# Optimization experiments

Hardware: AMD Instinct MI355X
Metric: run time of the kernel (lower is better)

Reference implementation:

```python
import jax, jax.numpy as jnp
import numpy as np

N_SUPPORT = 4096
N_QUERY = 8192
H = W = 28
IN_DIM = H * W  # 784
EMBED_DIM = 512
N_CLASSES = 64


def setup_inputs() -> dict:
    key = jax.random.key(0)
    k1, k2, k3, k4 = jax.random.split(key, 4)
    support_set = jax.random.normal(k1, (N_SUPPORT, 1, H, W), dtype=jnp.float32)
    query_set = jax.random.normal(k2, (N_QUERY, 1, H, W), dtype=jnp.float32)
    # one-hot support labels (N, C)
    lbl = jax.random.randint(k3, (N_SUPPORT,), 0, N_CLASSES)
    support_labels = jax.nn.one_hot(lbl, N_CLASSES, dtype=jnp.float32)
    # encoder params: flatten + dense projection stand-in for embedding_net
    W_enc = jax.random.normal(k4, (IN_DIM, EMBED_DIM), dtype=jnp.float32) * (1.0 / np.sqrt(IN_DIM))
    b_enc = jnp.zeros((EMBED_DIM,), dtype=jnp.float32)
    return {
        "support_set": support_set,
        "query_set": query_set,
        "support_labels": support_labels,
        "W_enc": W_enc,
        "b_enc": b_enc,
    }


def _encode(x, W_enc, b_enc):
    # (B, 1, H, W) -> (B, D): flatten + linear projection
    B = x.shape[0]
    return x.reshape(B, -1) @ W_enc + b_enc


def _neg_cdist(q, s):
    # -euclidean distance, computed via the expansion ||q-s||^2 = |q|^2 + |s|^2 - 2 q.s
    q2 = jnp.sum(q * q, axis=-1, keepdims=True)          # (Q, 1)
    s2 = jnp.sum(s * s, axis=-1)[None, :]                # (1, N)
    qs = jnp.einsum("qd,nd->qn", q, s)                  # (Q, N)
    d2 = jnp.maximum(q2 + s2 - 2.0 * qs, 0.0)
    return -jnp.sqrt(d2)


def reference(support_set, query_set, support_labels, W_enc, b_enc):
    support_emb = _encode(support_set, W_enc, b_enc)     # (N, D)
    query_emb = _encode(query_set, W_enc, b_enc)         # (Q, D)
    distances = _neg_cdist(query_emb, support_emb)       # (Q, N)
    attention = jax.nn.softmax(distances, axis=1)        # (Q, N)
    predictions = attention @ support_labels             # (Q, C)
    return predictions
```

## Files before the change

### kernel.cpp

```cpp
#include <hip/hip_runtime.h>

#define N_SUP 4096
#define N_QRY 8192
#define IN_DIM 784
#define EMB 512
#define NCLS 64
#define M_TOT (N_SUP + N_QRY)
#define NCHUNK 25
#define XCH 13

typedef _Float16 f16;
typedef _Float16 f16x8 __attribute__((ext_vector_type(8)));
typedef float f32x4 __attribute__((ext_vector_type(4)));

#define GLDS16(gp, lp)                                                        \
    __builtin_amdgcn_global_load_lds(                                         \
        (const __attribute__((address_space(1))) void*)(gp),                  \
        (__attribute__((address_space(3))) void*)(lp), 16, 0, 0)

static __device__ __forceinline__ f16x8 cvt8(const float* p) {
    float4 a = *(const float4*)p;
    float4 b = *(const float4*)(p + 4);
    f16x8 v;
    v[0] = (f16)a.x; v[1] = (f16)a.y; v[2] = (f16)a.z; v[3] = (f16)a.w;
    v[4] = (f16)b.x; v[5] = (f16)b.y; v[6] = (f16)b.z; v[7] = (f16)b.w;
    return v;
}

__global__ __launch_bounds__(256) void prep_wb(const float* __restrict__ W,
                                               f16* __restrict__ Wb) {
    int g = blockIdx.x * 256 + threadIdx.x;
    if (g >= NCHUNK * 32 * 64) return;
    int chunk = g >> 11;
    int rem = g & 2047;
    int nbg = rem >> 6, lane = rem & 63;
    int n = nbg * 16 + (lane & 15);
    int kbase = chunk * 32 + (lane >> 4) * 8;
    f16x8 v;
#pragma unroll
    for (int j = 0; j < 8; ++j) {
        int k = kbase + j;
        v[j] = (k < IN_DIM) ? (f16)W[(size_t)k * EMB + n] : (f16)0.f;
    }
    *(f16x8*)(Wb + (size_t)g * 8) = v;
}

__global__ __launch_bounds__(256) void prep_lbl(const float* __restrict__ lab,
                                                int* __restrict__ lbl) {
    const int w = threadIdx.x >> 6, lane = threadIdx.x & 63;
    const int s = blockIdx.x * 4 + w;
    float v = lab[(size_t)s * NCLS + lane];
    int c = lane;
#pragma unroll
    for (int off = 1; off < 64; off <<= 1) {
        float v2 = __shfl_xor(v, off);
        int c2 = __shfl_xor(c, off);
        if (v2 > v || (v2 == v && c2 < c)) { v = v2; c = c2; }
    }
    if (lane == 0) lbl[s] = c;
}

__global__ __launch_bounds__(256) void prep_L(const int* __restrict__ lbl,
                                              f16* __restrict__ Lcs) {
    int idx = blockIdx.x * 256 + threadIdx.x;
    if (idx >= NCLS * N_SUP) return;
    int c = idx >> 12, s = idx & (N_SUP - 1);
    Lcs[idx] = (lbl[s] == c) ? (f16)1.f : (f16)0.f;
}

__global__ __launch_bounds__(256) void prep_sb(const f16* __restrict__ E,
                                               f16* __restrict__ Sb) {
    int g = blockIdx.x * 256 + threadIdx.x;
    int s = g >> 6, lg = g & 63;
    f16x8 v = *(const f16x8*)(E + (size_t)s * EMB + lg * 8);
    *(f16x8*)(Sb + (size_t)s * EMB + ((lg ^ (s & 15)) * 8)) = v;
}

__global__ __launch_bounds__(256) void encode(
    const float* __restrict__ sup, const float* __restrict__ qry,
    const f16* __restrict__ Wb, const float* __restrict__ bias,
    f16* __restrict__ E, float* __restrict__ norms)
{
    __shared__ __align__(16) f16 Xs[32][72];
    const int tid = threadIdx.x;
    const int w = tid >> 6, lane = tid & 63;
    const int q = lane >> 4, c16 = lane & 15;
    const int mb = blockIdx.x >> 1;
    const int ch = blockIdx.x & 1;
    const int m0 = mb * 32;
    const int rbase = (w & 1) * 16;
    const int nbg0 = ch * 16 + (w >> 1) * 8;
    const int cbase = nbg0 * 16;

    f32x4 acc[8];
#pragma unroll
    for (int nb = 0; nb < 8; ++nb) acc[nb] = (f32x4){0.f, 0.f, 0.f, 0.f};

    const int sr = tid >> 3;
    const int sq = tid & 7;
    const float* xrow;
    {
        int gr = m0 + sr;
        xrow = (gr < N_SUP) ? sup + (size_t)gr * IN_DIM
                            : qry + (size_t)(gr - N_SUP) * IN_DIM;
    }

    f16x8 xg = cvt8(xrow + sq * 8);

    for (int c = 0; c < XCH; ++c) {
        __syncthreads();
        *(f16x8*)&Xs[sr][sq * 8] = xg;
        __syncthreads();
        if (c + 1 < XCH) {
            int k = (c + 1) * 64 + sq * 8;
            xg = (k + 8 <= IN_DIM) ? cvt8(xrow + k) : (f16x8){0,0,0,0,0,0,0,0};
        }
#pragma unroll
        for (int kc = 0; kc < 2; ++kc) {
            int c32 = c * 2 + kc;
            if (c32 >= NCHUNK) break;
            f16x8 a = *(const f16x8*)&Xs[rbase + c16][kc * 32 + q * 8];
            const f16* wb = Wb + ((size_t)(c32 * 32 + nbg0) * 64 + lane) * 8;
#pragma unroll
            for (int nb = 0; nb < 8; ++nb) {
                f16x8 b = *(const f16x8*)(wb + (size_t)nb * 512);
                acc[nb] = __builtin_amdgcn_mfma_f32_16x16x32_f16(a, b, acc[nb], 0, 0, 0);
            }
        }
    }

    float nrm[4] = {0.f, 0.f, 0.f, 0.f};
#pragma unroll
    for (int nb = 0; nb < 8; ++nb) {
        int col = cbase + nb * 16 + c16;
        float bv = bias[col];
#pragma unroll
        for (int r = 0; r < 4; ++r) {
            int row = m0 + rbase + q * 4 + r;
            float v = acc[nb][r] + bv;
            E[(size_t)row * EMB + col] = (f16)v;
            nrm[r] += v * v;
        }
    }
#pragma unroll
    for (int r = 0; r < 4; ++r) {
        float v = nrm[r];
        v += __shfl_xor(v, 1); v += __shfl_xor(v, 2);
        v += __shfl_xor(v, 4); v += __shfl_xor(v, 8);
        if (c16 == 0) atomicAdd(&norms[m0 + rbase + q * 4 + r], v);
    }
}

__global__ __launch_bounds__(256) void anchor(const f16* __restrict__ E,
                                              const float* __restrict__ norms,
                                              float* __restrict__ manc) {
    const int w = threadIdx.x >> 6, lane = threadIdx.x & 63;
    const int qrow = blockIdx.x * 4 + w;
    f16x8 qv = *(const f16x8*)(E + (size_t)(N_SUP + qrow) * EMB + lane * 8);
    f16x8 sv = *(const f16x8*)(E + lane * 8);
    float dot = 0.f;
#pragma unroll
    for (int j = 0; j < 8; ++j) dot += (float)qv[j] * (float)sv[j];
    dot += __shfl_xor(dot, 1);  dot += __shfl_xor(dot, 2);
    dot += __shfl_xor(dot, 4);  dot += __shfl_xor(dot, 8);
    dot += __shfl_xor(dot, 16); dot += __shfl_xor(dot, 32);
    if (lane == 0) {
        float d2 = fmaxf(norms[N_SUP + qrow] + norms[0] - 2.f * dot, 0.f);
        manc[qrow] = sqrtf(d2);
    }
}

__global__ __launch_bounds__(256, 3) void attn(
    const f16* __restrict__ E, const float* __restrict__ norms,
    const float* __restrict__ manc, const f16* __restrict__ Lcs,
    const f16* __restrict__ Sb, float* __restrict__ Num)
{
    __shared__ __align__(16) f16 Ss[2][16 * EMB];
    __shared__ __align__(16) f16 Pt[4][16][40];
    __shared__ float Sn[512];
    const int tid = threadIdx.x;
    const int w = tid >> 6, lane = tid & 63;
    const int q = lane >> 4, c16 = lane & 15;
    const int ss = blockIdx.x & 7;
    const int qt = blockIdx.x >> 3;

    Sn[tid]       = norms[ss * 512 + tid];
    Sn[256 + tid] = norms[ss * 512 + 256 + tid];

    f16x8 qf[16];
    const f16* qb = E + (size_t)(N_SUP + qt * 64 + w * 16 + c16) * EMB + q * 8;
#pragma unroll
    for (int ks = 0; ks < 16; ++ks) qf[ks] = *(const f16x8*)(qb + ks * 32);
    float q2[4], mrow[4];
#pragma unroll
    for (int r = 0; r < 4; ++r) {
        q2[r]   = norms[N_SUP + qt * 64 + w * 16 + q * 4 + r];
        mrow[r] = manc[qt * 64 + w * 16 + q * 4 + r];
    }

    f32x4 accPL[4];
#pragma unroll
    for (int nb = 0; nb < 4; ++nb) accPL[nb] = (f32x4){0.f, 0.f, 0.f, 0.f};

    const f16* sb_base = Sb + (size_t)(ss * 512) * EMB;
    const int wslot = w * 256;

#pragma unroll
    for (int i = 0; i < 4; ++i)
        GLDS16(sb_base + (size_t)(wslot + i * 64 + lane) * 8,
               &Ss[0][(wslot + i * 64) * 8]);
    __syncthreads();

#pragma unroll 2
    for (int t = 0; t < 32; ++t) {
        const int cur = t & 1;
        if (t + 1 < 32) {
            const f16* gsrc = sb_base + (size_t)(t + 1) * 16 * EMB;
#pragma unroll
            for (int i = 0; i < 4; ++i)
                GLDS16(gsrc + (size_t)(wslot + i * 64 + lane) * 8,
                       &Ss[cur ^ 1][(wslot + i * 64) * 8]);
        }
        f16x8 bl[4];
        if (t & 1) {
            const int ps0 = ss * 512 + (t >> 1) * 32;
#pragma unroll
            for (int nbc = 0; nbc < 4; ++nbc)
                bl[nbc] = *(const f16x8*)(Lcs + (size_t)(nbc * 16 + c16) * N_SUP + ps0 + q * 8);
        }

        f32x4 accQK = (f32x4){0.f, 0.f, 0.f, 0.f};
#pragma unroll
        for (int kc = 0; kc < 4; ++kc) {
#pragma unroll
            for (int ksl = 0; ksl < 4; ++ksl) {
                const int lg = kc * 16 + ksl * 4 + q;
                f16x8 b = *(const f16x8*)&Ss[cur][c16 * EMB + ((lg ^ c16) * 8)];
                accQK = __builtin_amdgcn_mfma_f32_16x16x32_f16(
                    qf[kc * 4 + ksl], b, accQK, 0, 0, 0);
            }
        }
        {
            const float s2 = Sn[t * 16 + c16];
            const int pcol = (t & 1) * 16 + c16;
#pragma unroll
            for (int r = 0; r < 4; ++r) {
                float d2 = fmaxf(q2[r] + s2 - 2.f * accQK[r], 0.f);
                float p = __expf(mrow[r] - __builtin_amdgcn_sqrtf(d2));
                p = fminf(p, 60000.f);
                Pt[w][q * 4 + r][pcol] = (f16)p;
            }
        }
        if (t & 1) {
            f16x8 af = *(const f16x8*)&Pt[w][c16][q * 8];
#pragma unroll
            for (int nbc = 0; nbc < 4; ++nbc)
                accPL[nbc] = __builtin_amdgcn_mfma_f32_16x16x32_f16(af, bl[nbc], accPL[nbc], 0, 0, 0);
        }

        __syncthreads();
    }

#pragma unroll
    for (int nbc = 0; nbc < 4; ++nbc)
#pragma unroll
        for (int r = 0; r < 4; ++r)
            atomicAdd(&Num[(size_t)(qt * 64 + w * 16 + q * 4 + r) * NCLS + nbc * 16 + c16],
                      accPL[nbc][r]);
}

__global__ __launch_bounds__(256) void finalize(const float* __restrict__ Num,
                                                float* __restrict__ out) {
    const int tid = threadIdx.x;
    const int w = tid >> 6, lane = tid & 63;
    const int qrow = blockIdx.x * 4 + w;
    float v = Num[(size_t)qrow * NCLS + lane];
    float s = v;
    s += __shfl_xor(s, 1);  s += __shfl_xor(s, 2);  s += __shfl_xor(s, 4);
    s += __shfl_xor(s, 8);  s += __shfl_xor(s, 16); s += __shfl_xor(s, 32);
    out[(size_t)qrow * NCLS + lane] = v / s;
}

extern "C" void kernel_launch(void* const* d_in, const int* in_sizes, int n_in,
                              void* d_out, int out_size, void* d_ws, size_t ws_size,
                              hipStream_t stream) {
    (void)in_sizes; (void)n_in; (void)out_size; (void)ws_size;
    const float* sup  = (const float*)d_in[0];
    const float* qry  = (const float*)d_in[1];
    const float* lab  = (const float*)d_in[2];
    const float* Wenc = (const float*)d_in[3];
    const float* benc = (const float*)d_in[4];
    float* out = (float*)d_out;

    char* ws = (char*)d_ws;
    size_t off = 0;
    f16* Wb = (f16*)(ws + off);        off += (size_t)NCHUNK * 32 * 64 * 8 * 2;
    f16* E  = (f16*)(ws + off);        off += (size_t)M_TOT * EMB * 2;
    f16* Sb = (f16*)(ws + off);        off += (size_t)N_SUP * EMB * 2;
    int* lbl = (int*)(ws + off);       off += (size_t)N_SUP * 4;
    f16* Lcs = (f16*)(ws + off);       off += (size_t)NCLS * N_SUP * 2;
    float* manc = (float*)(ws + off);  off += (size_t)N_QRY * 4;
    float* norms = (float*)(ws + off); off += (size_t)M_TOT * 4;
    float* Num = (float*)(ws + off);   off += (size_t)N_QRY * NCLS * 4;

    hipMemsetAsync(norms, 0, (size_t)M_TOT * 4 + (size_t)N_QRY * NCLS * 4, stream);

    prep_wb<<<(NCHUNK * 32 * 64 + 255) / 256, 256, 0, stream>>>(Wenc, Wb);
    prep_lbl<<<N_SUP / 4, 256, 0, stream>>>(lab, lbl);
    prep_L<<<NCLS * N_SUP / 256, 256, 0, stream>>>(lbl, Lcs);
    encode<<<M_TOT / 32 * 2, 256, 0, stream>>>(sup, qry, Wb, benc, E, norms);
    prep_sb<<<N_SUP * 64 / 256, 256, 0, stream>>>(E, Sb);
    anchor<<<N_QRY / 4, 256, 0, stream>>>(E, norms, manc);
    attn<<<N_QRY / 64 * 8, 256, 0, stream>>>(E, norms, manc, Lcs, Sb, Num);
    finalize<<<N_QRY / 4, 256, 0, stream>>>(Num, out);
}
```

Measured before the change: 199.3 us.

## Merge prep kernels into two launches and split QK MFMA accumulators

Folds the five small prep kernels into two multi-role launches (pre_enc, post_enc), cutting launch overhead and the gaps between kernels. In attn, the QK MFMA chain is split into two independent accumulators to shorten the dependency chain, and the section is wrapped in s_setprio. Wave 3 now reads its B fragments directly from global memory (Sb) rather than LDS, which is meant to ease LDS bandwidth pressure but adds global-load latency on that wave.

```diff
diff --git a/kernel.cpp b/kernel.cpp
--- a/kernel.cpp
+++ b/kernel.cpp
@@ -27,53 +27,38 @@
     return v;
 }
 
-__global__ __launch_bounds__(256) void prep_wb(const float* __restrict__ W,
-                                               f16* __restrict__ Wb) {
-    int g = blockIdx.x * 256 + threadIdx.x;
-    if (g >= NCHUNK * 32 * 64) return;
-    int chunk = g >> 11;
-    int rem = g & 2047;
-    int nbg = rem >> 6, lane = rem & 63;
-    int n = nbg * 16 + (lane & 15);
-    int kbase = chunk * 32 + (lane >> 4) * 8;
-    f16x8 v;
-#pragma unroll
-    for (int j = 0; j < 8; ++j) {
-        int k = kbase + j;
-        v[j] = (k < IN_DIM) ? (f16)W[(size_t)k * EMB + n] : (f16)0.f;
-    }
-    *(f16x8*)(Wb + (size_t)g * 8) = v;
-}
-
-__global__ __launch_bounds__(256) void prep_lbl(const float* __restrict__ lab,
-                                                int* __restrict__ lbl) {
-    const int w = threadIdx.x >> 6, lane = threadIdx.x & 63;
-    const int s = blockIdx.x * 4 + w;
-    float v = lab[(size_t)s * NCLS + lane];
-    int c = lane;
-#pragma unroll
-    for (int off = 1; off < 64; off <<= 1) {
-        float v2 = __shfl_xor(v, off);
-        int c2 = __shfl_xor(c, off);
-        if (v2 > v || (v2 == v && c2 < c)) { v = v2; c = c2; }
-    }
-    if (lane == 0) lbl[s] = c;
-}
-
-__global__ __launch_bounds__(256) void prep_L(const int* __restrict__ lbl,
-                                              f16* __restrict__ Lcs) {
-    int idx = blockIdx.x * 256 + threadIdx.x;
-    if (idx >= NCLS * N_SUP) return;
-    int c = idx >> 12, s = idx & (N_SUP - 1);
-    Lcs[idx] = (lbl[s] == c) ? (f16)1.f : (f16)0.f;
-}
-
-__global__ __launch_bounds__(256) void prep_sb(const f16* __restrict__ E,
-                                               f16* __restrict__ Sb) {
-    int g = blockIdx.x * 256 + threadIdx.x;
-    int s = g >> 6, lg = g & 63;
-    f16x8 v = *(const f16x8*)(E + (size_t)s * EMB + lg * 8);
-    *(f16x8*)(Sb + (size_t)s * EMB + ((lg ^ (s & 15)) * 8)) = v;
+__global__ __launch_bounds__(256) void pre_enc(const float* __restrict__ W,
+                                               const float* __restrict__ lab,
+                                               f16* __restrict__ Wb,
+                                               int* __restrict__ lbl) {
+    if (blockIdx.x < 200) {
+        int g = blockIdx.x * 256 + threadIdx.x;
+        if (g >= NCHUNK * 32 * 64) return;
+        int chunk = g >> 11;
+        int rem = g & 2047;
+        int nbg = rem >> 6, lane = rem & 63;
+        int n = nbg * 16 + (lane & 15);
+        int kbase = chunk * 32 + (lane >> 4) * 8;
+        f16x8 v;
+#pragma unroll
+        for (int j = 0; j < 8; ++j) {
+            int k = kbase + j;
+            v[j] = (k < IN_DIM) ? (f16)W[(size_t)k * EMB + n] : (f16)0.f;
+        }
+        *(f16x8*)(Wb + (size_t)g * 8) = v;
+    } else {
+        const int w = threadIdx.x >> 6, lane = threadIdx.x & 63;
+        const int s = (blockIdx.x - 200) * 4 + w;
+        float v = lab[(size_t)s * NCLS + lane];
+        int c = lane;
+#pragma unroll
+        for (int off = 1; off < 64; off <<= 1) {
+            float v2 = __shfl_xor(v, off);
+            int c2 = __shfl_xor(c, off);
+            if (v2 > v || (v2 == v && c2 < c)) { v = v2; c = c2; }
+        }
+        if (lane == 0) lbl[s] = c;
+    }
 }
 
 __global__ __launch_bounds__(256) void encode(
@@ -151,24 +136,54 @@
     }
 }
 
-__global__ __launch_bounds__(256) void anchor(const f16* __restrict__ E,
-                                              const float* __restrict__ norms,
-                                              float* __restrict__ manc) {
-    const int w = threadIdx.x >> 6, lane = threadIdx.x & 63;
-    const int qrow = blockIdx.x * 4 + w;
-    f16x8 qv = *(const f16x8*)(E + (size_t)(N_SUP + qrow) * EMB + lane * 8);
-    f16x8 sv = *(const f16x8*)(E + lane * 8);
-    float dot = 0.f;
-#pragma unroll
-    for (int j = 0; j < 8; ++j) dot += (float)qv[j] * (float)sv[j];
-    dot += __shfl_xor(dot, 1);  dot += __shfl_xor(dot, 2);
-    dot += __shfl_xor(dot, 4);  dot += __shfl_xor(dot, 8);
-    dot += __shfl_xor(dot, 16); dot += __shfl_xor(dot, 32);
-    if (lane == 0) {
-        float d2 = fmaxf(norms[N_SUP + qrow] + norms[0] - 2.f * dot, 0.f);
-        manc[qrow] = sqrtf(d2);
-    }
-}
+__global__ __launch_bounds__(256) void post_enc(
+    const f16* __restrict__ E, const float* __restrict__ norms,
+    const int* __restrict__ lbl, f16* __restrict__ Sb,
+    f16* __restrict__ Lcs, float* __restrict__ manc)
+{
+    const int b = blockIdx.x;
+    if (b < 1024) {
+        int g = b * 256 + threadIdx.x;
+        int s = g >> 6, lg = g & 63;
+        f16x8 v = *(const f16x8*)(E + (size_t)s * EMB + lg * 8);
+        *(f16x8*)(Sb + (size_t)s * EMB + ((lg ^ (s & 15)) * 8)) = v;
+    } else if (b < 3072) {
+        const int w = threadIdx.x >> 6, lane = threadIdx.x & 63;
+        const int qrow = (b - 1024) * 4 + w;
+        f16x8 qv = *(const f16x8*)(E + (size_t)(N_SUP + qrow) * EMB + lane * 8);
+        f16x8 sv = *(const f16x8*)(E + lane * 8);
+        float dot = 0.f;
+#pragma unroll
+        for (int j = 0; j < 8; ++j) dot += (float)qv[j] * (float)sv[j];
+        dot += __shfl_xor(dot, 1);  dot += __shfl_xor(dot, 2);
+        dot += __shfl_xor(dot, 4);  dot += __shfl_xor(dot, 8);
+        dot += __shfl_xor(dot, 16); dot += __shfl_xor(dot, 32);
+        if (lane == 0) {
+            float d2 = fmaxf(norms[N_SUP + qrow] + norms[0] - 2.f * dot, 0.f);
+            manc[qrow] = sqrtf(d2);
+        }
+    } else {
+        int idx = (b - 3072) * 256 + threadIdx.x;
+        int c = idx >> 12, s = idx & (N_SUP - 1);
+        Lcs[idx] = (lbl[s] == c) ? (f16)1.f : (f16)0.f;
+    }
+}
+
+#define QK_BODY(bsrc, a0, a1)                                                 \
+    _Pragma("unroll")                                                         \
+    for (int kc = 0; kc < 4; ++kc) {                                          \
+        _Pragma("unroll")                                                     \
+        for (int ksl = 0; ksl < 4; ++ksl) {                                   \
+            const int lg = kc * 16 + ksl * 4 + q;                             \
+            f16x8 bfr = *(const f16x8*)&(bsrc)[c16 * EMB + ((lg ^ c16) * 8)]; \
+            if (ksl & 1)                                                      \
+                a1 = __builtin_amdgcn_mfma_f32_16x16x32_f16(                  \
+                    qf[kc * 4 + ksl], bfr, a1, 0, 0, 0);                      \
+            else                                                              \
+                a0 = __builtin_amdgcn_mfma_f32_16x16x32_f16(                  \
+                    qf[kc * 4 + ksl], bfr, a0, 0, 0, 0);                      \
+        }                                                                     \
+    }
 
 __global__ __launch_bounds__(256, 3) void attn(
     const f16* __restrict__ E, const float* __restrict__ norms,
@@ -229,17 +244,19 @@
                 bl[nbc] = *(const f16x8*)(Lcs + (size_t)(nbc * 16 + c16) * N_SUP + ps0 + q * 8);
         }
 
-        f32x4 accQK = (f32x4){0.f, 0.f, 0.f, 0.f};
-#pragma unroll
-        for (int kc = 0; kc < 4; ++kc) {
-#pragma unroll
-            for (int ksl = 0; ksl < 4; ++ksl) {
-                const int lg = kc * 16 + ksl * 4 + q;
-                f16x8 b = *(const f16x8*)&Ss[cur][c16 * EMB + ((lg ^ c16) * 8)];
-                accQK = __builtin_amdgcn_mfma_f32_16x16x32_f16(
-                    qf[kc * 4 + ksl], b, accQK, 0, 0, 0);
-            }
-        }
+        f32x4 a0 = (f32x4){0.f, 0.f, 0.f, 0.f};
+        f32x4 a1 = (f32x4){0.f, 0.f, 0.f, 0.f};
+        __builtin_amdgcn_s_setprio(1);
+        if (w == 3) {
+            const f16* bsrc = sb_base + (size_t)t * 16 * EMB;
+            QK_BODY(bsrc, a0, a1)
+        } else {
+            const f16* bsrc = &Ss[cur][0];
+            QK_BODY(bsrc, a0, a1)
+        }
+        __builtin_amdgcn_s_setprio(0);
+        f32x4 accQK = a0 + a1;
+
         {
             const float s2 = Sn[t * 16 + c16];
             const int pcol = (t & 1) * 16 + c16;
@@ -305,12 +322,9 @@
 
     hipMemsetAsync(norms, 0, (size_t)M_TOT * 4 + (size_t)N_QRY * NCLS * 4, stream);
 
-    prep_wb<<<(NCHUNK * 32 * 64 + 255) / 256, 256, 0, stream>>>(Wenc, Wb);
-    prep_lbl<<<N_SUP / 4, 256, 0, stream>>>(lab, lbl);
-    prep_L<<<NCLS * N_SUP / 256, 256, 0, stream>>>(lbl, Lcs);
+    pre_enc<<<1224, 256, 0, stream>>>(Wenc, lab, Wb, lbl);
     encode<<<M_TOT / 32 * 2, 256, 0, stream>>>(sup, qry, Wb, benc, E, norms);
-    prep_sb<<<N_SUP * 64 / 256, 256, 0, stream>>>(E, Sb);
-    anchor<<<N_QRY / 4, 256, 0, stream>>>(E, norms, manc);
+    post_enc<<<4096, 256, 0, stream>>>(E, norms, lbl, Sb, Lcs, manc);
     attn<<<N_QRY / 64 * 8, 256, 0, stream>>>(E, norms, manc, Lcs, Sb, Num);
     finalize<<<N_QRY / 4, 256, 0, stream>>>(Num, out);
 }
```

New measurement: 532.6 us. +167.2%, slower.
